# Kernel optimization log

Hardware: AMD Instinct MI355X
Metric: run time of the kernel (lower is better)

Reference implementation:

```python
import jax, jax.numpy as jnp
import numpy as np

BETA = 0.9
THRESHOLD = 1.0
SLOPE = 10.0


def setup_inputs() -> dict:
    key = jax.random.key(0)
    ks = jax.random.split(key, 5)
    B, T, F, H = 32768, 10, 256, 512
    x = jax.random.normal(ks[0], (B, T, F), dtype=jnp.float32)
    W1 = jax.random.normal(ks[1], (H, F), dtype=jnp.float32) * (1.0 / np.sqrt(F))
    b1 = jax.random.normal(ks[2], (H,), dtype=jnp.float32) * 0.01
    W2 = jax.random.normal(ks[3], (1, H), dtype=jnp.float32) * (1.0 / np.sqrt(H))
    b2 = jax.random.normal(ks[4], (1,), dtype=jnp.float32) * 0.01
    return {"x": x, "W1": W1, "b1": b1, "W2": W2, "b2": b2}


def _surrogate_spike(mem):
    return jax.nn.sigmoid(SLOPE * (mem - THRESHOLD))


def _lif(cur, mem):
    mem = BETA * mem + cur
    spike = _surrogate_spike(mem)
    mem = mem - spike * THRESHOLD
    return spike, mem


def reference(x, W1, b1, W2, b2):
    B, T, F = x.shape
    H = W1.shape[0]
    # Precompute fc1 over all time steps in one big GEMM: [B,T,H]
    cur1_all = jnp.einsum('btf,hf->bth', x, W1) + b1

    mem1_0 = jnp.zeros((B, H), dtype=x.dtype)
    mem2_0 = jnp.zeros((B, 1), dtype=x.dtype)

    def step(carry, cur1_t):
        mem1, mem2 = carry
        spk1, mem1 = _lif(cur1_t, mem1)
        cur2 = spk1 @ W2.T + b2  # [B,1]
        spk2, mem2 = _lif(cur2, mem2)
        return (mem1, mem2), spk2

    # scan over the fixed 10 time steps (hard sequential dependency on mem)
    (_, _), spk2_seq = jax.lax.scan(step, (mem1_0, mem2_0),
                                    jnp.moveaxis(cur1_all, 1, 0))  # [T,B,1]
    spk_mean = jnp.sum(spk2_seq, axis=0) / 10.0
    return jax.nn.sigmoid(spk_mean)
```

## Files before the change

kernel.cpp:

```cpp
#include <hip/hip_runtime.h>
#include <hip/hip_bf16.h>


typedef short short8 __attribute__((ext_vector_type(8)));
typedef float f32x4 __attribute__((ext_vector_type(4)));

__device__ __forceinline__ unsigned short bfbits(float f) {
  union { __hip_bfloat16 h; unsigned short u; } c;
  c.h = __float2bfloat16(f);
  return c.u;
}

__device__ __forceinline__ unsigned int bfpack(float a, float b) {
  return (unsigned int)bfbits(a) | ((unsigned int)bfbits(b) << 16);
}

__device__ __forceinline__ float fast_sigmoid(float z) {
  float e = __expf(-z);
  return __builtin_amdgcn_rcpf(1.0f + e);
}

__device__ __forceinline__ void lif4(f32x4& mv, const f32x4 av, float w2c, float pr[4]) {
#pragma unroll
  for (int e = 0; e < 4; ++e) {
    float m   = fmaf(mv[e], 0.9f, av[e]);
    float spk = fast_sigmoid(fmaf(m, 10.f, -10.f));
    mv[e] = m - spk;
    pr[e] = fmaf(spk, w2c, pr[e]);
  }
}

__global__ void w1_to_bf16(const float* __restrict__ w1, unsigned short* __restrict__ o) {
  int i = blockIdx.x * 256 + threadIdx.x;
  float4 v = reinterpret_cast<const float4*>(w1)[i];
  reinterpret_cast<uint2*>(o)[i] = make_uint2(bfpack(v.x, v.y), bfpack(v.z, v.w));
}

__device__ __forceinline__ short8 cvt_frag(const float* p) {
  const float4 v0 = *reinterpret_cast<const float4*>(p);
  const float4 v1 = *reinterpret_cast<const float4*>(p + 4);
  union { unsigned int u[4]; short8 s; } cv;
  cv.u[0] = bfpack(v0.x, v0.y);
  cv.u[1] = bfpack(v0.z, v0.w);
  cv.u[2] = bfpack(v1.x, v1.y);
  cv.u[3] = bfpack(v1.z, v1.w);
  return cv.s;
}

template <bool USE_WS>
__global__
__attribute__((amdgpu_flat_work_group_size(512, 512)))
void snn_main(const float* __restrict__ x,
              const unsigned short* __restrict__ w1bf,
              const float* __restrict__ w1f,
              const float* __restrict__ b1,
              const float* __restrict__ w2,
              const float* __restrict__ b2,
              float* __restrict__ out)
{
  __shared__ __align__(16) float mem_lds[8][512][4];
  __shared__ __align__(16) unsigned short xt[2][2][32][132];
  __shared__ float cur2_lds[10][32][9];

  const int tid  = threadIdx.x;
  const int lane = tid & 63;
  const int wave = tid >> 6;
  const int l15  = lane & 15;
  const int lq   = lane >> 4;
  const long b0  = (long)blockIdx.x * 32;
  const int h0   = wave * 64;

  float w2l[4], b1l[4];
#pragma unroll
  for (int ct = 0; ct < 4; ++ct) {
    int h = h0 + ct * 16 + l15;
    w2l[ct] = w2[h];
    b1l[ct] = b1[h];
  }

#pragma unroll
  for (int p = 0; p < 8; ++p) {
    f32x4 z = {0.f, 0.f, 0.f, 0.f};
    *reinterpret_cast<f32x4*>(&mem_lds[p][tid][0]) = z;
  }

  const int sr = tid >> 4;
  const int sc = tid & 15;
  const float* xrow = x + (b0 + sr) * 2560;

  const unsigned short* wb = w1bf + (h0 + l15) * 256 + lq * 8;
  const float*          wf = w1f  + (h0 + l15) * 256 + lq * 8;

  uint2 pf[4];
#pragma unroll
  for (int j = 0; j < 4; ++j) {
    const float4 v = *reinterpret_cast<const float4*>(xrow + (sc + j * 16) * 4);
    pf[j] = make_uint2(bfpack(v.x, v.y), bfpack(v.z, v.w));
  }

#pragma unroll 1
  for (int t = 0; t < 10; ++t) {
    const int par = t & 1;
#pragma unroll
    for (int j = 0; j < 4; ++j)
      *reinterpret_cast<uint2*>(
          &xt[par][j >> 1][sr][(sc + (j & 1) * 16) * 4]) = pf[j];
    {
      const int tn = (t < 9) ? t + 1 : 9;
#pragma unroll
      for (int j = 0; j < 4; ++j) {
        const float4 v = *reinterpret_cast<const float4*>(
            xrow + tn * 256 + (sc + j * 16) * 4);
        pf[j] = make_uint2(bfpack(v.x, v.y), bfpack(v.z, v.w));
      }
    }
    short8 bfr0[4];
#pragma unroll
    for (int c = 0; c < 4; ++c) {
      if constexpr (USE_WS) bfr0[c] = *reinterpret_cast<const short8*>(wb + c * 4096);
      else                  bfr0[c] = cvt_frag(wf + c * 4096);
    }
    __syncthreads();

    f32x4 acc[2][4];
#pragma unroll
    for (int rt = 0; rt < 2; ++rt)
#pragma unroll
      for (int c = 0; c < 4; ++c) {
        f32x4 cc = { b1l[c], b1l[c], b1l[c], b1l[c] };
        acc[rt][c] = cc;
      }

#pragma unroll
    for (int kk = 0; kk < 8; ++kk) {
      short8 a[2], bfr[4];
#pragma unroll
      for (int rt = 0; rt < 2; ++rt)
        a[rt] = *reinterpret_cast<const short8*>(
            &xt[par][kk >> 2][rt * 16 + l15][(kk & 3) * 32 + lq * 8]);
      if (kk == 0) {
#pragma unroll
        for (int c = 0; c < 4; ++c) bfr[c] = bfr0[c];
      } else {
#pragma unroll
        for (int c = 0; c < 4; ++c) {
          if constexpr (USE_WS)
            bfr[c] = *reinterpret_cast<const short8*>(wb + c * 4096 + kk * 32);
          else
            bfr[c] = cvt_frag(wf + c * 4096 + kk * 32);
        }
      }
#pragma unroll
      for (int rt = 0; rt < 2; ++rt)
#pragma unroll
        for (int c = 0; c < 4; ++c)
          acc[rt][c] = __builtin_amdgcn_mfma_f32_16x16x32_bf16(a[rt], bfr[c], acc[rt][c], 0, 0, 0);
    }

#pragma unroll
    for (int rt = 0; rt < 2; ++rt) {
      float pr[4] = {0.f, 0.f, 0.f, 0.f};
#pragma unroll
      for (int c = 0; c < 4; ++c) {
        const int p = rt * 4 + c;
        f32x4* slot = reinterpret_cast<f32x4*>(&mem_lds[p][tid][0]);
        f32x4 mv = *slot;
        lif4(mv, acc[rt][c], w2l[c], pr);
        *slot = mv;
      }
#pragma unroll
      for (int e = 0; e < 4; ++e) {
        float v = pr[e];
        v += __shfl_xor(v, 1); v += __shfl_xor(v, 2);
        v += __shfl_xor(v, 4); v += __shfl_xor(v, 8);
        if (l15 == 0) cur2_lds[t][rt * 16 + lq * 4 + e][wave] = v;
      }
    }
  }

  __syncthreads();

  if (tid < 32) {
    const float bias2 = b2[0];
    float mem2 = 0.f, spksum = 0.f;
#pragma unroll
    for (int t = 0; t < 10; ++t) {
      float c2 = bias2;
#pragma unroll
      for (int w = 0; w < 8; ++w) c2 += cur2_lds[t][tid][w];
      float m   = fmaf(mem2, 0.9f, c2);
      float spk = fast_sigmoid(fmaf(m, 10.f, -10.f));
      mem2   = m - spk;
      spksum += spk;
    }
    out[b0 + tid] = fast_sigmoid(spksum * 0.1f);
  }
}

extern "C" void kernel_launch(void* const* d_in, const int* in_sizes, int n_in,
                              void* d_out, int out_size, void* d_ws, size_t ws_size,
                              hipStream_t stream) {
  const float* x  = (const float*)d_in[0];
  const float* W1 = (const float*)d_in[1];
  const float* b1 = (const float*)d_in[2];
  const float* W2 = (const float*)d_in[3];
  const float* b2 = (const float*)d_in[4];
  float* out = (float*)d_out;
  (void)in_sizes; (void)n_in;

  const int grid = out_size / 32;

  if (ws_size >= 512 * 256 * sizeof(unsigned short)) {
    unsigned short* w1bf = (unsigned short*)d_ws;
    w1_to_bf16<<<128, 256, 0, stream>>>(W1, w1bf);
    snn_main<true><<<grid, 512, 0, stream>>>(x, w1bf, W1, b1, W2, b2, out);
  } else {
    snn_main<false><<<grid, 512, 0, stream>>>(x, nullptr, W1, b1, W2, b2, out);
  }
}
```

Baseline: 177.6 us.

## Split hidden dim across 16 waves with 1024-thread blocks and raise MFMA priority

Doubles the block to 1024 threads so each wave covers 32 hidden units instead of 64, halving per-thread accumulators, LIF state and weight fragments. The cross-wave cur2 reduction widens to 16 partials, and s_setprio brackets the MFMA loop. It also drops the early prefetch of the first weight fragment ahead of the barrier. The aim is more waves per CU to hide x-load and LDS latency, at the cost of more barrier participants and more reduction work.

```diff
diff --git a/kernel.cpp b/kernel.cpp
--- a/kernel.cpp
+++ b/kernel.cpp
@@ -49,7 +49,7 @@
 
 template <bool USE_WS>
 __global__
-__attribute__((amdgpu_flat_work_group_size(512, 512)))
+__attribute__((amdgpu_flat_work_group_size(1024, 1024)))
 void snn_main(const float* __restrict__ x,
               const unsigned short* __restrict__ w1bf,
               const float* __restrict__ w1f,
@@ -58,9 +58,9 @@
               const float* __restrict__ b2,
               float* __restrict__ out)
 {
-  __shared__ __align__(16) float mem_lds[8][512][4];
+  __shared__ __align__(16) float mem_lds[4][1024][4];
   __shared__ __align__(16) unsigned short xt[2][2][32][132];
-  __shared__ float cur2_lds[10][32][9];
+  __shared__ float cur2_lds[10][32][17];
 
   const int tid  = threadIdx.x;
   const int lane = tid & 63;
@@ -68,101 +68,89 @@
   const int l15  = lane & 15;
   const int lq   = lane >> 4;
   const long b0  = (long)blockIdx.x * 32;
-  const int h0   = wave * 64;
-
-  float w2l[4], b1l[4];
-#pragma unroll
-  for (int ct = 0; ct < 4; ++ct) {
-    int h = h0 + ct * 16 + l15;
-    w2l[ct] = w2[h];
-    b1l[ct] = b1[h];
-  }
-
-#pragma unroll
-  for (int p = 0; p < 8; ++p) {
+  const int h0   = wave * 32;
+
+  float w2l[2], b1l[2];
+#pragma unroll
+  for (int c = 0; c < 2; ++c) {
+    int h = h0 + c * 16 + l15;
+    w2l[c] = w2[h];
+    b1l[c] = b1[h];
+  }
+
+#pragma unroll
+  for (int p = 0; p < 4; ++p) {
     f32x4 z = {0.f, 0.f, 0.f, 0.f};
     *reinterpret_cast<f32x4*>(&mem_lds[p][tid][0]) = z;
   }
 
-  const int sr = tid >> 4;
-  const int sc = tid & 15;
+  const int sr = tid >> 5;
+  const int sc = tid & 31;
   const float* xrow = x + (b0 + sr) * 2560;
 
   const unsigned short* wb = w1bf + (h0 + l15) * 256 + lq * 8;
   const float*          wf = w1f  + (h0 + l15) * 256 + lq * 8;
 
-  uint2 pf[4];
-#pragma unroll
-  for (int j = 0; j < 4; ++j) {
-    const float4 v = *reinterpret_cast<const float4*>(xrow + (sc + j * 16) * 4);
-    pf[j] = make_uint2(bfpack(v.x, v.y), bfpack(v.z, v.w));
+  uint2 pf[2];
+  {
+    const float4 v0 = *reinterpret_cast<const float4*>(xrow + sc * 4);
+    const float4 v1 = *reinterpret_cast<const float4*>(xrow + 128 + sc * 4);
+    pf[0] = make_uint2(bfpack(v0.x, v0.y), bfpack(v0.z, v0.w));
+    pf[1] = make_uint2(bfpack(v1.x, v1.y), bfpack(v1.z, v1.w));
   }
 
 #pragma unroll 1
   for (int t = 0; t < 10; ++t) {
     const int par = t & 1;
-#pragma unroll
-    for (int j = 0; j < 4; ++j)
-      *reinterpret_cast<uint2*>(
-          &xt[par][j >> 1][sr][(sc + (j & 1) * 16) * 4]) = pf[j];
+    *reinterpret_cast<uint2*>(&xt[par][0][sr][sc * 4]) = pf[0];
+    *reinterpret_cast<uint2*>(&xt[par][1][sr][sc * 4]) = pf[1];
     {
       const int tn = (t < 9) ? t + 1 : 9;
-#pragma unroll
-      for (int j = 0; j < 4; ++j) {
-        const float4 v = *reinterpret_cast<const float4*>(
-            xrow + tn * 256 + (sc + j * 16) * 4);
-        pf[j] = make_uint2(bfpack(v.x, v.y), bfpack(v.z, v.w));
-      }
-    }
-    short8 bfr0[4];
-#pragma unroll
-    for (int c = 0; c < 4; ++c) {
-      if constexpr (USE_WS) bfr0[c] = *reinterpret_cast<const short8*>(wb + c * 4096);
-      else                  bfr0[c] = cvt_frag(wf + c * 4096);
+      const float4 v0 = *reinterpret_cast<const float4*>(xrow + tn * 256 + sc * 4);
+      const float4 v1 = *reinterpret_cast<const float4*>(xrow + tn * 256 + 128 + sc * 4);
+      pf[0] = make_uint2(bfpack(v0.x, v0.y), bfpack(v0.z, v0.w));
+      pf[1] = make_uint2(bfpack(v1.x, v1.y), bfpack(v1.z, v1.w));
     }
     __syncthreads();
 
-    f32x4 acc[2][4];
+    f32x4 acc[2][2];
 #pragma unroll
     for (int rt = 0; rt < 2; ++rt)
 #pragma unroll
-      for (int c = 0; c < 4; ++c) {
+      for (int c = 0; c < 2; ++c) {
         f32x4 cc = { b1l[c], b1l[c], b1l[c], b1l[c] };
         acc[rt][c] = cc;
       }
 
+    __builtin_amdgcn_s_setprio(1);
 #pragma unroll
     for (int kk = 0; kk < 8; ++kk) {
-      short8 a[2], bfr[4];
+      short8 a[2], bfr[2];
 #pragma unroll
       for (int rt = 0; rt < 2; ++rt)
         a[rt] = *reinterpret_cast<const short8*>(
             &xt[par][kk >> 2][rt * 16 + l15][(kk & 3) * 32 + lq * 8]);
-      if (kk == 0) {
-#pragma unroll
-        for (int c = 0; c < 4; ++c) bfr[c] = bfr0[c];
-      } else {
-#pragma unroll
-        for (int c = 0; c < 4; ++c) {
-          if constexpr (USE_WS)
-            bfr[c] = *reinterpret_cast<const short8*>(wb + c * 4096 + kk * 32);
-          else
-            bfr[c] = cvt_frag(wf + c * 4096 + kk * 32);
-        }
+#pragma unroll
+      for (int c = 0; c < 2; ++c) {
+        if constexpr (USE_WS)
+          bfr[c] = *reinterpret_cast<const short8*>(wb + c * 4096 + kk * 32);
+        else
+          bfr[c] = cvt_frag(wf + c * 4096 + kk * 32);
       }
 #pragma unroll
       for (int rt = 0; rt < 2; ++rt)
 #pragma unroll
-        for (int c = 0; c < 4; ++c)
+        for (int c = 0; c < 2; ++c)
           acc[rt][c] = __builtin_amdgcn_mfma_f32_16x16x32_bf16(a[rt], bfr[c], acc[rt][c], 0, 0, 0);
     }
+    __builtin_amdgcn_s_setprio(0);
 
 #pragma unroll
     for (int rt = 0; rt < 2; ++rt) {
       float pr[4] = {0.f, 0.f, 0.f, 0.f};
 #pragma unroll
-      for (int c = 0; c < 4; ++c) {
-        const int p = rt * 4 + c;
+      for (int c = 0; c < 2; ++c) {
+        const int p = rt * 2 + c;
         f32x4* slot = reinterpret_cast<f32x4*>(&mem_lds[p][tid][0]);
         f32x4 mv = *slot;
         lif4(mv, acc[rt][c], w2l[c], pr);
@@ -187,7 +175,7 @@
     for (int t = 0; t < 10; ++t) {
       float c2 = bias2;
 #pragma unroll
-      for (int w = 0; w < 8; ++w) c2 += cur2_lds[t][tid][w];
+      for (int w = 0; w < 16; ++w) c2 += cur2_lds[t][tid][w];
       float m   = fmaf(mem2, 0.9f, c2);
       float spk = fast_sigmoid(fmaf(m, 10.f, -10.f));
       mem2   = m - spk;
@@ -213,8 +201,8 @@
   if (ws_size >= 512 * 256 * sizeof(unsigned short)) {
     unsigned short* w1bf = (unsigned short*)d_ws;
     w1_to_bf16<<<128, 256, 0, stream>>>(W1, w1bf);
-    snn_main<true><<<grid, 512, 0, stream>>>(x, w1bf, W1, b1, W2, b2, out);
+    snn_main<true><<<grid, 1024, 0, stream>>>(x, w1bf, W1, b1, W2, b2, out);
   } else {
-    snn_main<false><<<grid, 512, 0, stream>>>(x, nullptr, W1, b1, W2, b2, out);
-  }
-}
+    snn_main<false><<<grid, 1024, 0, stream>>>(x, nullptr, W1, b1, W2, b2, out);
+  }
+}
```

Measured after the change: 183.6 us. 3.4% more time.
